# Optimization experiments

Measured on AMD Instinct MI355X. Metric: run time of the kernel, lower is better.

Reference implementation:

```python
import jax, jax.numpy as jnp
import numpy as np

B, S, D, F, E, K = 2, 1024, 2048, 1024, 8, 2


def setup_inputs() -> dict:
    key = jax.random.key(0)
    ks = jax.random.split(key, 5)
    scale_x = 0.02
    return {
        "x": jax.random.normal(ks[0], (B, S, D), dtype=jnp.float32),
        "w_router": jax.random.normal(ks[1], (E, D), dtype=jnp.float32) * scale_x,
        "w_gate": jax.random.normal(ks[2], (E, F, D), dtype=jnp.float32) * scale_x,
        "w_up": jax.random.normal(ks[3], (E, F, D), dtype=jnp.float32) * scale_x,
        "w_down": jax.random.normal(ks[4], (E, D, F), dtype=jnp.float32) * scale_x,
        "top_k": K,
    }


def reference(x, w_router, w_gate, w_up, w_down, top_k):
    # Router: logits [B,S,E] -> top-k indices + softmax over top-k logits (fp32)
    logits = jnp.einsum("bsd,ed->bse", x, w_router)
    top_logits, top_idx = jax.lax.top_k(logits, top_k)          # [B,S,K]
    gates = jax.nn.softmax(top_logits.astype(jnp.float32), axis=-1)
    # SwitchGLU: per-expert gated MLP. Compute all experts densely, then gather
    # the selected expert output per token (reference-faithful math).
    h = jax.nn.silu(jnp.einsum("bsd,efd->besf", x, w_gate)) * jnp.einsum(
        "bsd,efd->besf", x, w_up
    )                                                            # [B,E,S,F]
    out_all = jnp.einsum("besf,edf->bsed", h, w_down)            # [B,S,E,D]
    y = jnp.take_along_axis(out_all, top_idx[..., None], axis=2)  # [B,S,K,D]
    return (y * gates[..., None].astype(y.dtype)).sum(axis=-2)   # [B,S,D]
```

## Files before the change

kernel.cpp:

```cpp
#include <hip/hip_runtime.h>
#include <hip/hip_bf16.h>

#define T_TOK 2048
#define DIM   2048
#define FFN   1024
#define NE    8

typedef __attribute__((ext_vector_type(8))) short bf16x8;
typedef __attribute__((ext_vector_type(4))) float f32x4;

__device__ __forceinline__ unsigned short f2bf(float f) {
  __hip_bfloat16 h = __float2bfloat16(f);
  return __builtin_bit_cast(unsigned short, h);
}

__device__ __forceinline__ void gload_lds16(const unsigned short* g, unsigned short* l) {
  __builtin_amdgcn_global_load_lds(
      (const __attribute__((address_space(1))) void*)g,
      (__attribute__((address_space(3))) void*)l, 16, 0, 0);
}

__global__ void cvt_f32_to_bf16(const float* __restrict__ in,
                                unsigned short* __restrict__ out, int n4) {
  int i = blockIdx.x * blockDim.x + threadIdx.x;
  int stride = gridDim.x * blockDim.x;
  for (; i < n4; i += stride) {
    float4 v = reinterpret_cast<const float4*>(in)[i];
    ushort4 o;
    o.x = f2bf(v.x); o.y = f2bf(v.y); o.z = f2bf(v.z); o.w = f2bf(v.w);
    reinterpret_cast<ushort4*>(out)[i] = o;
  }
}

__global__ __launch_bounds__(256) void router_topk(
    const float* __restrict__ x, const float* __restrict__ wr,
    int* __restrict__ top_i, float* __restrict__ top_g) {
  int t = blockIdx.x * 4 + (threadIdx.x >> 6);
  int lane = threadIdx.x & 63;
  const float4* xr = reinterpret_cast<const float4*>(x) + (size_t)t * (DIM / 4);
  const float4* wrv = reinterpret_cast<const float4*>(wr);
  float acc[NE];
#pragma unroll
  for (int e = 0; e < NE; ++e) acc[e] = 0.f;
#pragma unroll
  for (int it = 0; it < DIM / 4 / 64; ++it) {
    int d4 = it * 64 + lane;
    float4 xv = xr[d4];
#pragma unroll
    for (int e = 0; e < NE; ++e) {
      float4 wv = wrv[e * (DIM / 4) + d4];
      acc[e] += xv.x * wv.x + xv.y * wv.y + xv.z * wv.z + xv.w * wv.w;
    }
  }
#pragma unroll
  for (int off = 32; off > 0; off >>= 1) {
#pragma unroll
    for (int e = 0; e < NE; ++e) acc[e] += __shfl_xor(acc[e], off, 64);
  }
  if (lane == 0) {
    int i0 = 0; float m0 = acc[0];
#pragma unroll
    for (int e = 1; e < NE; ++e) if (acc[e] > m0) { m0 = acc[e]; i0 = e; }
    int i1 = -1; float m1 = -3.4e38f;
#pragma unroll
    for (int e = 0; e < NE; ++e) if (e != i0 && acc[e] > m1) { m1 = acc[e]; i1 = e; }
    float tv = expf(m1 - m0);
    float den = 1.f + tv;
    top_i[t * 2 + 0] = i0; top_i[t * 2 + 1] = i1;
    top_g[t * 2 + 0] = 1.f / den; top_g[t * 2 + 1] = tv / den;
  }
}

__global__ void count_offsets(const int* __restrict__ top_i,
                              int* __restrict__ offs, int* __restrict__ cursor) {
  __shared__ int cnt[NE];
  if (threadIdx.x < NE) cnt[threadIdx.x] = 0;
  __syncthreads();
  for (int i = threadIdx.x; i < T_TOK * 2; i += blockDim.x) atomicAdd(&cnt[top_i[i]], 1);
  __syncthreads();
  if (threadIdx.x == 0) {
    int s = 0;
    for (int e = 0; e < NE; ++e) { offs[e] = s; cursor[e] = s; s += cnt[e]; }
    offs[NE] = s;
  }
}

__global__ void scatter_tokens(const int* __restrict__ top_i, const float* __restrict__ top_g,
                               int* __restrict__ cursor, int* __restrict__ tok_list,
                               float* __restrict__ gate_lst, int* __restrict__ slot_lst) {
  int t = blockIdx.x * blockDim.x + threadIdx.x;
  if (t >= T_TOK) return;
#pragma unroll
  for (int s = 0; s < 2; ++s) {
    int e = top_i[t * 2 + s];
    int p = atomicAdd(&cursor[e], 1);
    tok_list[p] = t;
    gate_lst[p] = top_g[t * 2 + s];
    slot_lst[p] = s;
  }
}

__global__ __launch_bounds__(256, 2) void gateup_gemm(
    const unsigned short* __restrict__ xb, const unsigned short* __restrict__ wgb,
    const unsigned short* __restrict__ wub, const int* __restrict__ tok_list,
    const int* __restrict__ offs, unsigned short* __restrict__ hbuf) {
  const int e = blockIdx.z;
  const int row0 = offs[e];
  const int n_e = offs[e + 1] - row0;
  const int mt = blockIdx.y;
  if (mt * 64 >= n_e) return;
  const int nt = blockIdx.x;

  __shared__ unsigned short As[64 * 64];
  __shared__ unsigned short Bg[128 * 64];
  __shared__ unsigned short Bu[128 * 64];

  const int tid = threadIdx.x;
  const int wid = tid >> 6;
  const int lane = tid & 63;

  const int gchunk = (((lane & 7) ^ ((lane >> 3) & 7)) << 3);

  const unsigned short* gA[2];
  unsigned short* lA[2];
#pragma unroll
  for (int p = 0; p < 2; ++p) {
    int rt = wid * 16 + p * 8 + (lane >> 3);
    int ar = mt * 64 + rt; if (ar >= n_e) ar = n_e - 1;
    gA[p] = xb + (size_t)tok_list[row0 + ar] * DIM + gchunk;
    lA[p] = &As[(wid * 16 + p * 8) * 64];
  }
  const size_t wbase = (size_t)e * FFN * DIM + (size_t)(nt * 128) * DIM;
  const unsigned short* gG[4];
  const unsigned short* gU[4];
  unsigned short* lG[4];
  unsigned short* lU[4];
#pragma unroll
  for (int p = 0; p < 4; ++p) {
    int rt = wid * 32 + p * 8 + (lane >> 3);
    gG[p] = wgb + wbase + (size_t)rt * DIM + gchunk;
    gU[p] = wub + wbase + (size_t)rt * DIM + gchunk;
    lG[p] = &Bg[(wid * 32 + p * 8) * 64];
    lU[p] = &Bu[(wid * 32 + p * 8) * 64];
  }

  f32x4 accg[2][4];
  f32x4 accu[2][4];
#pragma unroll
  for (int i = 0; i < 2; ++i)
#pragma unroll
    for (int j = 0; j < 4; ++j) {
      accg[i][j] = (f32x4){0.f, 0.f, 0.f, 0.f};
      accu[i][j] = (f32x4){0.f, 0.f, 0.f, 0.f};
    }

  const int warow = (wid >> 1) * 32;
  const int wacol = (wid & 1) * 64;
  const int frow = lane & 15;
  const int eo0 = ((((0 << 2) + (lane >> 4)) ^ (lane & 7)) << 3);
  const int eo1 = ((((1 << 2) + (lane >> 4)) ^ (lane & 7)) << 3);

  for (int k0 = 0; k0 < DIM; k0 += 64) {
#pragma unroll
    for (int p = 0; p < 2; ++p) gload_lds16(gA[p] + k0, lA[p]);
#pragma unroll
    for (int p = 0; p < 4; ++p) gload_lds16(gG[p] + k0, lG[p]);
#pragma unroll
    for (int p = 0; p < 4; ++p) gload_lds16(gU[p] + k0, lU[p]);
    __syncthreads();
#pragma unroll
    for (int kk = 0; kk < 2; ++kk) {
      const int eo = kk ? eo1 : eo0;
      bf16x8 af[2], bg[4], bu[4];
#pragma unroll
      for (int i = 0; i < 2; ++i)
        af[i] = *reinterpret_cast<const bf16x8*>(&As[(warow + i * 16 + frow) * 64 + eo]);
#pragma unroll
      for (int j = 0; j < 4; ++j) {
        bg[j] = *reinterpret_cast<const bf16x8*>(&Bg[(wacol + j * 16 + frow) * 64 + eo]);
        bu[j] = *reinterpret_cast<const bf16x8*>(&Bu[(wacol + j * 16 + frow) * 64 + eo]);
      }
#pragma unroll
      for (int i = 0; i < 2; ++i)
#pragma unroll
        for (int j = 0; j < 4; ++j) {
          accg[i][j] = __builtin_amdgcn_mfma_f32_16x16x32_bf16(af[i], bg[j], accg[i][j], 0, 0, 0);
          accu[i][j] = __builtin_amdgcn_mfma_f32_16x16x32_bf16(af[i], bu[j], accu[i][j], 0, 0, 0);
        }
    }
    __syncthreads();
  }

#pragma unroll
  for (int i = 0; i < 2; ++i) {
#pragma unroll
    for (int jj = 0; jj < 4; ++jj) {
      int r = mt * 64 + warow + i * 16 + (lane >> 4) * 4 + jj;
      if (r < n_e) {
#pragma unroll
        for (int j = 0; j < 4; ++j) {
          float g = accg[i][j][jj];
          float u = accu[i][j][jj];
          float h = (g / (1.f + __expf(-g))) * u;
          int f = nt * 128 + wacol + j * 16 + (lane & 15);
          hbuf[(size_t)(row0 + r) * FFN + f] = f2bf(h);
        }
      }
    }
  }
}

__global__ __launch_bounds__(256, 4) void down_gemm(
    const unsigned short* __restrict__ hbuf, const unsigned short* __restrict__ wdb,
    const int* __restrict__ tok_list, const float* __restrict__ gate_lst,
    const int* __restrict__ slot_lst, const int* __restrict__ offs,
    float* __restrict__ yslots) {
  const int e = blockIdx.z;
  const int row0 = offs[e];
  const int n_e = offs[e + 1] - row0;
  const int mt = blockIdx.y;
  if (mt * 64 >= n_e) return;
  const int nt = blockIdx.x;

  __shared__ unsigned short As[64 * 64];
  __shared__ unsigned short Bs[128 * 64];

  const int tid = threadIdx.x;
  const int wid = tid >> 6;
  const int lane = tid & 63;

  const int gchunk = (((lane & 7) ^ ((lane >> 3) & 7)) << 3);

  const unsigned short* gA[2];
  unsigned short* lA[2];
#pragma unroll
  for (int p = 0; p < 2; ++p) {
    int rt = wid * 16 + p * 8 + (lane >> 3);
    int ar = mt * 64 + rt; if (ar >= n_e) ar = n_e - 1;
    gA[p] = hbuf + (size_t)(row0 + ar) * FFN + gchunk;
    lA[p] = &As[(wid * 16 + p * 8) * 64];
  }
  const unsigned short* gB[4];
  unsigned short* lB[4];
#pragma unroll
  for (int p = 0; p < 4; ++p) {
    int rt = wid * 32 + p * 8 + (lane >> 3);
    gB[p] = wdb + ((size_t)e * DIM + nt * 128 + rt) * FFN + gchunk;
    lB[p] = &Bs[(wid * 32 + p * 8) * 64];
  }

  f32x4 acc[2][4];
#pragma unroll
  for (int i = 0; i < 2; ++i)
#pragma unroll
    for (int j = 0; j < 4; ++j) acc[i][j] = (f32x4){0.f, 0.f, 0.f, 0.f};

  const int warow = (wid >> 1) * 32;
  const int wacol = (wid & 1) * 64;
  const int frow = lane & 15;
  const int eo0 = ((((0 << 2) + (lane >> 4)) ^ (lane & 7)) << 3);
  const int eo1 = ((((1 << 2) + (lane >> 4)) ^ (lane & 7)) << 3);

  for (int k0 = 0; k0 < FFN; k0 += 64) {
#pragma unroll
    for (int p = 0; p < 2; ++p) gload_lds16(gA[p] + k0, lA[p]);
#pragma unroll
    for (int p = 0; p < 4; ++p) gload_lds16(gB[p] + k0, lB[p]);
    __syncthreads();
#pragma unroll
    for (int kk = 0; kk < 2; ++kk) {
      const int eo = kk ? eo1 : eo0;
      bf16x8 af[2], bf[4];
#pragma unroll
      for (int i = 0; i < 2; ++i)
        af[i] = *reinterpret_cast<const bf16x8*>(&As[(warow + i * 16 + frow) * 64 + eo]);
#pragma unroll
      for (int j = 0; j < 4; ++j)
        bf[j] = *reinterpret_cast<const bf16x8*>(&Bs[(wacol + j * 16 + frow) * 64 + eo]);
#pragma unroll
      for (int i = 0; i < 2; ++i)
#pragma unroll
        for (int j = 0; j < 4; ++j)
          acc[i][j] = __builtin_amdgcn_mfma_f32_16x16x32_bf16(af[i], bf[j], acc[i][j], 0, 0, 0);
    }
    __syncthreads();
  }

#pragma unroll
  for (int i = 0; i < 2; ++i) {
#pragma unroll
    for (int jj = 0; jj < 4; ++jj) {
      int r = mt * 64 + warow + i * 16 + (lane >> 4) * 4 + jj;
      if (r < n_e) {
        int tk = tok_list[row0 + r];
        float gt = gate_lst[row0 + r];
        int sl = slot_lst[row0 + r];
        float* yrow = yslots + ((size_t)sl * T_TOK + tk) * DIM;
#pragma unroll
        for (int j = 0; j < 4; ++j) {
          int d = nt * 128 + wacol + j * 16 + (lane & 15);
          yrow[d] = gt * acc[i][j][jj];
        }
      }
    }
  }
}

__global__ void combine(const float* __restrict__ y, float* __restrict__ out) {
  int i = blockIdx.x * blockDim.x + threadIdx.x;
  int stride = gridDim.x * blockDim.x;
  const float4* y0 = reinterpret_cast<const float4*>(y);
  const float4* y1 = reinterpret_cast<const float4*>(y + (size_t)T_TOK * DIM);
  float4* o = reinterpret_cast<float4*>(out);
  for (; i < T_TOK * DIM / 4; i += stride) {
    float4 a = y0[i], b = y1[i];
    float4 r;
    r.x = a.x + b.x; r.y = a.y + b.y; r.z = a.z + b.z; r.w = a.w + b.w;
    o[i] = r;
  }
}

extern "C" void kernel_launch(void* const* d_in, const int* in_sizes, int n_in,
                              void* d_out, int out_size, void* d_ws, size_t ws_size,
                              hipStream_t stream) {
  const float* x = (const float*)d_in[0];
  const float* wr = (const float*)d_in[1];
  const float* wg = (const float*)d_in[2];
  const float* wu = (const float*)d_in[3];
  const float* wd = (const float*)d_in[4];
  float* out = (float*)d_out;

  char* ws = (char*)d_ws;
  size_t off = 0;
  auto alloc = [&](size_t bytes) {
    char* p = ws + off;
    off += (bytes + 255) & ~(size_t)255;
    return p;
  };
  unsigned short* xb   = (unsigned short*)alloc((size_t)T_TOK * DIM * 2);
  unsigned short* wgb  = (unsigned short*)alloc((size_t)NE * FFN * DIM * 2);
  unsigned short* wub  = (unsigned short*)alloc((size_t)NE * FFN * DIM * 2);
  unsigned short* wdb  = (unsigned short*)alloc((size_t)NE * DIM * FFN * 2);
  unsigned short* hbuf = (unsigned short*)alloc((size_t)T_TOK * 2 * FFN * 2);
  float* yslots        = (float*)alloc((size_t)2 * T_TOK * DIM * 4);
  int* top_i     = (int*)alloc(T_TOK * 2 * 4);
  float* top_g   = (float*)alloc(T_TOK * 2 * 4);
  int* tok_list  = (int*)alloc(T_TOK * 2 * 4);
  float* gate_lst = (float*)alloc(T_TOK * 2 * 4);
  int* slot_lst  = (int*)alloc(T_TOK * 2 * 4);
  int* offs      = (int*)alloc(64);
  int* cursor    = (int*)alloc(64);
  if (off > ws_size) return;

  cvt_f32_to_bf16<<<2048, 256, 0, stream>>>(x, xb, T_TOK * DIM / 4);
  cvt_f32_to_bf16<<<4096, 256, 0, stream>>>(wg, wgb, NE * FFN * DIM / 4);
  cvt_f32_to_bf16<<<4096, 256, 0, stream>>>(wu, wub, NE * FFN * DIM / 4);
  cvt_f32_to_bf16<<<4096, 256, 0, stream>>>(wd, wdb, NE * DIM * FFN / 4);
  router_topk<<<T_TOK / 4, 256, 0, stream>>>(x, wr, top_i, top_g);
  count_offsets<<<1, 256, 0, stream>>>(top_i, offs, cursor);
  scatter_tokens<<<(T_TOK + 255) / 256, 256, 0, stream>>>(top_i, top_g, cursor, tok_list,
                                                          gate_lst, slot_lst);
  gateup_gemm<<<dim3(FFN / 128, 32, NE), 256, 0, stream>>>(xb, wgb, wub, tok_list, offs, hbuf);
  down_gemm<<<dim3(DIM / 128, 32, NE), 256, 0, stream>>>(hbuf, wdb, tok_list, gate_lst,
                                                         slot_lst, offs, yslots);
  combine<<<2048, 256, 0, stream>>>(yslots, out);
}
```

Before: 207.5 us.

## Fuse fp32 weight conversion into GEMM loads with double-buffered LDS pipeline

Removes the three separate weight-conversion kernels. The gate/up and down GEMMs now load fp32 weights directly into registers, convert them to bf16 and write them into swizzled LDS. Both GEMMs gain a two-stage LDS double buffer: the next tile's loads are issued before the current MFMAs and written to LDS afterwards. Each weight tile is now read as fp32 and converted repeatedly across the M-tiles, which costs more global traffic and VALU work. Register and LDS pressure also rise, and down_gemm occupancy drops to 3.

```diff
diff --git a/kernel.cpp b/kernel.cpp
--- a/kernel.cpp
+++ b/kernel.cpp
@@ -7,6 +7,7 @@
 #define NE    8
 
 typedef __attribute__((ext_vector_type(8))) short bf16x8;
+typedef __attribute__((ext_vector_type(8))) unsigned short u16x8;
 typedef __attribute__((ext_vector_type(4))) float f32x4;
 
 __device__ __forceinline__ unsigned short f2bf(float f) {
@@ -101,8 +102,8 @@
 }
 
 __global__ __launch_bounds__(256, 2) void gateup_gemm(
-    const unsigned short* __restrict__ xb, const unsigned short* __restrict__ wgb,
-    const unsigned short* __restrict__ wub, const int* __restrict__ tok_list,
+    const unsigned short* __restrict__ xb, const float* __restrict__ wg,
+    const float* __restrict__ wu, const int* __restrict__ tok_list,
     const int* __restrict__ offs, unsigned short* __restrict__ hbuf) {
   const int e = blockIdx.z;
   const int row0 = offs[e];
@@ -111,38 +112,57 @@
   if (mt * 64 >= n_e) return;
   const int nt = blockIdx.x;
 
-  __shared__ unsigned short As[64 * 64];
-  __shared__ unsigned short Bg[128 * 64];
-  __shared__ unsigned short Bu[128 * 64];
+  __shared__ unsigned short As[2][64 * 64];
+  __shared__ unsigned short Bg[2][128 * 64];
+  __shared__ unsigned short Bu[2][128 * 64];
 
   const int tid = threadIdx.x;
   const int wid = tid >> 6;
   const int lane = tid & 63;
 
   const int gchunk = (((lane & 7) ^ ((lane >> 3) & 7)) << 3);
-
   const unsigned short* gA[2];
-  unsigned short* lA[2];
+  int lAoff[2];
 #pragma unroll
   for (int p = 0; p < 2; ++p) {
     int rt = wid * 16 + p * 8 + (lane >> 3);
     int ar = mt * 64 + rt; if (ar >= n_e) ar = n_e - 1;
     gA[p] = xb + (size_t)tok_list[row0 + ar] * DIM + gchunk;
-    lA[p] = &As[(wid * 16 + p * 8) * 64];
-  }
-  const size_t wbase = (size_t)e * FFN * DIM + (size_t)(nt * 128) * DIM;
-  const unsigned short* gG[4];
-  const unsigned short* gU[4];
-  unsigned short* lG[4];
-  unsigned short* lU[4];
-#pragma unroll
-  for (int p = 0; p < 4; ++p) {
-    int rt = wid * 32 + p * 8 + (lane >> 3);
-    gG[p] = wgb + wbase + (size_t)rt * DIM + gchunk;
-    gU[p] = wub + wbase + (size_t)rt * DIM + gchunk;
-    lG[p] = &Bg[(wid * 32 + p * 8) * 64];
-    lU[p] = &Bu[(wid * 32 + p * 8) * 64];
-  }
+    lAoff[p] = (wid * 16 + p * 8) * 64;
+  }
+
+  const float* gGb = wg + ((size_t)e * FFN + nt * 128 + wid * 32 + (lane >> 3)) * DIM + (lane & 7) * 8;
+  const float* gUb = wu + ((size_t)e * FFN + nt * 128 + wid * 32 + (lane >> 3)) * DIM + (lane & 7) * 8;
+  const int lrow = wid * 32 + (lane >> 3);
+  const int wboff = lrow * 64 + ((lane & 7) ^ (lane >> 3)) * 8;
+
+  float Rg[4][8], Ru[4][8];
+
+  auto issueA = [&](int k0, int buf) {
+#pragma unroll
+    for (int p = 0; p < 2; ++p) gload_lds16(gA[p] + k0, &As[buf][lAoff[p]]);
+  };
+  auto issueB = [&](int k0) {
+#pragma unroll
+    for (int p = 0; p < 4; ++p) {
+      const float4* pg = reinterpret_cast<const float4*>(gGb + (size_t)p * 8 * DIM + k0);
+      const float4* pu = reinterpret_cast<const float4*>(gUb + (size_t)p * 8 * DIM + k0);
+      *reinterpret_cast<float4*>(&Rg[p][0]) = pg[0];
+      *reinterpret_cast<float4*>(&Rg[p][4]) = pg[1];
+      *reinterpret_cast<float4*>(&Ru[p][0]) = pu[0];
+      *reinterpret_cast<float4*>(&Ru[p][4]) = pu[1];
+    }
+  };
+  auto cvtWriteB = [&](int buf) {
+#pragma unroll
+    for (int p = 0; p < 4; ++p) {
+      u16x8 vg, vu;
+#pragma unroll
+      for (int q = 0; q < 8; ++q) { vg[q] = f2bf(Rg[p][q]); vu[q] = f2bf(Ru[p][q]); }
+      *reinterpret_cast<u16x8*>(&Bg[buf][wboff + p * 512]) = vg;
+      *reinterpret_cast<u16x8*>(&Bu[buf][wboff + p * 512]) = vu;
+    }
+  };
 
   f32x4 accg[2][4];
   f32x4 accu[2][4];
@@ -157,28 +177,29 @@
   const int warow = (wid >> 1) * 32;
   const int wacol = (wid & 1) * 64;
   const int frow = lane & 15;
-  const int eo0 = ((((0 << 2) + (lane >> 4)) ^ (lane & 7)) << 3);
-  const int eo1 = ((((1 << 2) + (lane >> 4)) ^ (lane & 7)) << 3);
-
-  for (int k0 = 0; k0 < DIM; k0 += 64) {
-#pragma unroll
-    for (int p = 0; p < 2; ++p) gload_lds16(gA[p] + k0, lA[p]);
-#pragma unroll
-    for (int p = 0; p < 4; ++p) gload_lds16(gG[p] + k0, lG[p]);
-#pragma unroll
-    for (int p = 0; p < 4; ++p) gload_lds16(gU[p] + k0, lU[p]);
-    __syncthreads();
+  const int eo0 = ((((lane >> 4)) ^ (lane & 7)) << 3);
+  const int eo1 = (((4 + (lane >> 4)) ^ (lane & 7)) << 3);
+
+  issueA(0, 0);
+  issueB(0);
+  cvtWriteB(0);
+  __syncthreads();
+
+  const int NT = DIM / 64;
+  int cur = 0;
+  for (int t = 0; t < NT; ++t) {
+    if (t + 1 < NT) { issueA((t + 1) * 64, cur ^ 1); issueB((t + 1) * 64); }
 #pragma unroll
     for (int kk = 0; kk < 2; ++kk) {
       const int eo = kk ? eo1 : eo0;
       bf16x8 af[2], bg[4], bu[4];
 #pragma unroll
       for (int i = 0; i < 2; ++i)
-        af[i] = *reinterpret_cast<const bf16x8*>(&As[(warow + i * 16 + frow) * 64 + eo]);
+        af[i] = *reinterpret_cast<const bf16x8*>(&As[cur][(warow + i * 16 + frow) * 64 + eo]);
 #pragma unroll
       for (int j = 0; j < 4; ++j) {
-        bg[j] = *reinterpret_cast<const bf16x8*>(&Bg[(wacol + j * 16 + frow) * 64 + eo]);
-        bu[j] = *reinterpret_cast<const bf16x8*>(&Bu[(wacol + j * 16 + frow) * 64 + eo]);
+        bg[j] = *reinterpret_cast<const bf16x8*>(&Bg[cur][(wacol + j * 16 + frow) * 64 + eo]);
+        bu[j] = *reinterpret_cast<const bf16x8*>(&Bu[cur][(wacol + j * 16 + frow) * 64 + eo]);
       }
 #pragma unroll
       for (int i = 0; i < 2; ++i)
@@ -188,7 +209,9 @@
           accu[i][j] = __builtin_amdgcn_mfma_f32_16x16x32_bf16(af[i], bu[j], accu[i][j], 0, 0, 0);
         }
     }
+    if (t + 1 < NT) cvtWriteB(cur ^ 1);
     __syncthreads();
+    cur ^= 1;
   }
 
 #pragma unroll
@@ -210,8 +233,8 @@
   }
 }
 
-__global__ __launch_bounds__(256, 4) void down_gemm(
-    const unsigned short* __restrict__ hbuf, const unsigned short* __restrict__ wdb,
+__global__ __launch_bounds__(256, 3) void down_gemm(
+    const unsigned short* __restrict__ hbuf, const float* __restrict__ wd,
     const int* __restrict__ tok_list, const float* __restrict__ gate_lst,
     const int* __restrict__ slot_lst, const int* __restrict__ offs,
     float* __restrict__ yslots) {
@@ -222,32 +245,51 @@
   if (mt * 64 >= n_e) return;
   const int nt = blockIdx.x;
 
-  __shared__ unsigned short As[64 * 64];
-  __shared__ unsigned short Bs[128 * 64];
+  __shared__ unsigned short As[2][64 * 64];
+  __shared__ unsigned short Bs[2][128 * 64];
 
   const int tid = threadIdx.x;
   const int wid = tid >> 6;
   const int lane = tid & 63;
 
   const int gchunk = (((lane & 7) ^ ((lane >> 3) & 7)) << 3);
-
   const unsigned short* gA[2];
-  unsigned short* lA[2];
+  int lAoff[2];
 #pragma unroll
   for (int p = 0; p < 2; ++p) {
     int rt = wid * 16 + p * 8 + (lane >> 3);
     int ar = mt * 64 + rt; if (ar >= n_e) ar = n_e - 1;
     gA[p] = hbuf + (size_t)(row0 + ar) * FFN + gchunk;
-    lA[p] = &As[(wid * 16 + p * 8) * 64];
-  }
-  const unsigned short* gB[4];
-  unsigned short* lB[4];
-#pragma unroll
-  for (int p = 0; p < 4; ++p) {
-    int rt = wid * 32 + p * 8 + (lane >> 3);
-    gB[p] = wdb + ((size_t)e * DIM + nt * 128 + rt) * FFN + gchunk;
-    lB[p] = &Bs[(wid * 32 + p * 8) * 64];
-  }
+    lAoff[p] = (wid * 16 + p * 8) * 64;
+  }
+
+  const float* gBb = wd + ((size_t)e * DIM + nt * 128 + wid * 32 + (lane >> 3)) * FFN + (lane & 7) * 8;
+  const int lrow = wid * 32 + (lane >> 3);
+  const int wboff = lrow * 64 + ((lane & 7) ^ (lane >> 3)) * 8;
+
+  float Rb[4][8];
+
+  auto issueA = [&](int k0, int buf) {
+#pragma unroll
+    for (int p = 0; p < 2; ++p) gload_lds16(gA[p] + k0, &As[buf][lAoff[p]]);
+  };
+  auto issueB = [&](int k0) {
+#pragma unroll
+    for (int p = 0; p < 4; ++p) {
+      const float4* pb = reinterpret_cast<const float4*>(gBb + (size_t)p * 8 * FFN + k0);
+      *reinterpret_cast<float4*>(&Rb[p][0]) = pb[0];
+      *reinterpret_cast<float4*>(&Rb[p][4]) = pb[1];
+    }
+  };
+  auto cvtWriteB = [&](int buf) {
+#pragma unroll
+    for (int p = 0; p < 4; ++p) {
+      u16x8 vb;
+#pragma unroll
+      for (int q = 0; q < 8; ++q) vb[q] = f2bf(Rb[p][q]);
+      *reinterpret_cast<u16x8*>(&Bs[buf][wboff + p * 512]) = vb;
+    }
+  };
 
   f32x4 acc[2][4];
 #pragma unroll
@@ -258,32 +300,37 @@
   const int warow = (wid >> 1) * 32;
   const int wacol = (wid & 1) * 64;
   const int frow = lane & 15;
-  const int eo0 = ((((0 << 2) + (lane >> 4)) ^ (lane & 7)) << 3);
-  const int eo1 = ((((1 << 2) + (lane >> 4)) ^ (lane & 7)) << 3);
-
-  for (int k0 = 0; k0 < FFN; k0 += 64) {
-#pragma unroll
-    for (int p = 0; p < 2; ++p) gload_lds16(gA[p] + k0, lA[p]);
-#pragma unroll
-    for (int p = 0; p < 4; ++p) gload_lds16(gB[p] + k0, lB[p]);
-    __syncthreads();
+  const int eo0 = ((((lane >> 4)) ^ (lane & 7)) << 3);
+  const int eo1 = (((4 + (lane >> 4)) ^ (lane & 7)) << 3);
+
+  issueA(0, 0);
+  issueB(0);
+  cvtWriteB(0);
+  __syncthreads();
+
+  const int NT = FFN / 64;
+  int cur = 0;
+  for (int t = 0; t < NT; ++t) {
+    if (t + 1 < NT) { issueA((t + 1) * 64, cur ^ 1); issueB((t + 1) * 64); }
 #pragma unroll
     for (int kk = 0; kk < 2; ++kk) {
       const int eo = kk ? eo1 : eo0;
       bf16x8 af[2], bf[4];
 #pragma unroll
       for (int i = 0; i < 2; ++i)
-        af[i] = *reinterpret_cast<const bf16x8*>(&As[(warow + i * 16 + frow) * 64 + eo]);
+        af[i] = *reinterpret_cast<const bf16x8*>(&As[cur][(warow + i * 16 + frow) * 64 + eo]);
 #pragma unroll
       for (int j = 0; j < 4; ++j)
-        bf[j] = *reinterpret_cast<const bf16x8*>(&Bs[(wacol + j * 16 + frow) * 64 + eo]);
+        bf[j] = *reinterpret_cast<const bf16x8*>(&Bs[cur][(wacol + j * 16 + frow) * 64 + eo]);
 #pragma unroll
       for (int i = 0; i < 2; ++i)
 #pragma unroll
         for (int j = 0; j < 4; ++j)
           acc[i][j] = __builtin_amdgcn_mfma_f32_16x16x32_bf16(af[i], bf[j], acc[i][j], 0, 0, 0);
     }
+    if (t + 1 < NT) cvtWriteB(cur ^ 1);
     __syncthreads();
+    cur ^= 1;
   }
 
 #pragma unroll
@@ -338,9 +385,6 @@
     return p;
   };
   unsigned short* xb   = (unsigned short*)alloc((size_t)T_TOK * DIM * 2);
-  unsigned short* wgb  = (unsigned short*)alloc((size_t)NE * FFN * DIM * 2);
-  unsigned short* wub  = (unsigned short*)alloc((size_t)NE * FFN * DIM * 2);
-  unsigned short* wdb  = (unsigned short*)alloc((size_t)NE * DIM * FFN * 2);
   unsigned short* hbuf = (unsigned short*)alloc((size_t)T_TOK * 2 * FFN * 2);
   float* yslots        = (float*)alloc((size_t)2 * T_TOK * DIM * 4);
   int* top_i     = (int*)alloc(T_TOK * 2 * 4);
@@ -353,15 +397,12 @@
   if (off > ws_size) return;
 
   cvt_f32_to_bf16<<<2048, 256, 0, stream>>>(x, xb, T_TOK * DIM / 4);
-  cvt_f32_to_bf16<<<4096, 256, 0, stream>>>(wg, wgb, NE * FFN * DIM / 4);
-  cvt_f32_to_bf16<<<4096, 256, 0, stream>>>(wu, wub, NE * FFN * DIM / 4);
-  cvt_f32_to_bf16<<<4096, 256, 0, stream>>>(wd, wdb, NE * DIM * FFN / 4);
   router_topk<<<T_TOK / 4, 256, 0, stream>>>(x, wr, top_i, top_g);
   count_offsets<<<1, 256, 0, stream>>>(top_i, offs, cursor);
   scatter_tokens<<<(T_TOK + 255) / 256, 256, 0, stream>>>(top_i, top_g, cursor, tok_list,
                                                           gate_lst, slot_lst);
-  gateup_gemm<<<dim3(FFN / 128, 32, NE), 256, 0, stream>>>(xb, wgb, wub, tok_list, offs, hbuf);
-  down_gemm<<<dim3(DIM / 128, 32, NE), 256, 0, stream>>>(hbuf, wdb, tok_list, gate_lst,
+  gateup_gemm<<<dim3(FFN / 128, 32, NE), 256, 0, stream>>>(xb, wg, wu, tok_list, offs, hbuf);
+  down_gemm<<<dim3(DIM / 128, 32, NE), 256, 0, stream>>>(hbuf, wd, tok_list, gate_lst,
                                                          slot_lst, offs, yslots);
   combine<<<2048, 256, 0, stream>>>(yslots, out);
 }
```

New measurement: 339.4 us. 1.64x slower.
